# Performance work log

Hardware: AMD Instinct MI355X
Metric: run time of the kernel (lower is better)

## Reference

```python
import jax, jax.numpy as jnp
import numpy as np

B, T, C, H = 32, 512, 8, 256  # batch, seq_len, n_channels, HIDDEN_SIZE
G = 4 * H  # gate dim (i, f, g, o)


def setup_inputs() -> dict:
    key = jax.random.key(0)
    ks = jax.random.split(key, 12)
    k_scale = 1.0 / np.sqrt(H)  # PyTorch LSTM/Linear uniform init bound
    u = lambda k, shape: jax.random.uniform(k, shape, jnp.float32, -k_scale, k_scale)
    return {
        "x": jax.random.normal(ks[0], (B, T, C), jnp.float32),
        # per-channel LSTM layer 1 (input_size=1)
        "Wih1": u(ks[1], (C, G, 1)),
        "Whh1": u(ks[2], (C, G, H)),
        "bih1": u(ks[3], (C, G)),
        "bhh1": u(ks[4], (C, G)),
        # per-channel LSTM layer 2 (input_size=H)
        "Wih2": u(ks[5], (C, G, H)),
        "Whh2": u(ks[6], (C, G, H)),
        "bih2": u(ks[7], (C, G)),
        "bhh2": u(ks[8], (C, G)),
        # per-channel Linear(H, 1)
        "Wlin": u(ks[9], (C, H)),
        "blin": u(ks[10], (C,)),
    }


def _lstm_layer(x_proj, Whh):
    """x_proj: [T, C, B, 4H] precomputed input projection + biases.
    Whh: [C, 4H, H]. Returns hidden states [T, C, B, H]."""
    c_dim, b_dim = x_proj.shape[1], x_proj.shape[2]
    h0 = jnp.zeros((c_dim, b_dim, H), x_proj.dtype)
    c0 = jnp.zeros((c_dim, b_dim, H), x_proj.dtype)

    def step(carry, xp_t):
        h, c = carry
        gates = xp_t + jnp.einsum('cbh,cgh->cbg', h, Whh)
        i, f, g, o = jnp.split(gates, 4, axis=-1)  # PyTorch gate order i,f,g,o
        i = jax.nn.sigmoid(i)
        f = jax.nn.sigmoid(f)
        g = jnp.tanh(g)
        o = jax.nn.sigmoid(o)
        c_new = f * c + i * g
        h_new = o * jnp.tanh(c_new)
        return (h_new, c_new), h_new

    _, hs = jax.lax.scan(step, (h0, c0), x_proj)
    return hs  # [T, C, B, H]


def reference(x, Wih1, Whh1, bih1, bhh1, Wih2, Whh2, bih2, bhh2, Wlin, blin):
    # Dropout layers are identity in eval mode.
    # Layer 1: input_size=1 -> input projection is a per-channel scale of x.
    b1 = (bih1 + bhh1)[None, :, None, :]  # [1, C, 1, 4H]
    xp1 = jnp.einsum('btc,cg->tcbg', x, Wih1[:, :, 0]) + b1  # [T, C, B, 4H]
    h1 = _lstm_layer(xp1, Whh1)  # [T, C, B, H]

    # Layer 2
    b2 = (bih2 + bhh2)[None, :, None, :]
    xp2 = jnp.einsum('tcbh,cgh->tcbg', h1, Wih2) + b2
    h2 = _lstm_layer(xp2, Whh2)  # [T, C, B, H]

    # Per-channel Linear(H, 1), concatenated over channel dim.
    out = jnp.einsum('tcbh,ch->btc', h2, Wlin) + blin[None, None, :]
    return out  # [B, T, C]
```

## Files before the change

kernel.cpp:

```cpp
#include <hip/hip_runtime.h>

#define Bn 32
#define Tn 512
#define Cn 8
#define Hn 256
#define Gn 1024
#define NTHR 256
#define SLC  16
#define NBLK (Cn*2*SLC)
#define K2n  (Hn/2)
#define BUFS 4
#define EXU  (BUFS*Cn*K2n*Bn)
#define GP2  18

typedef __attribute__((ext_vector_type(8))) __bf16 bf16x8;
typedef __attribute__((ext_vector_type(8))) short  short8;
typedef __attribute__((ext_vector_type(4))) float  f32x4;
typedef __attribute__((ext_vector_type(4))) unsigned uintx4;
typedef unsigned long long u64;

__device__ __forceinline__ unsigned bfr(float f) {
    unsigned u = __float_as_uint(f);
    return (u + 0x7fffu + ((u >> 16) & 1u)) >> 16;
}
__device__ __forceinline__ float sigmf(float v)  { return 1.0f / (1.0f + __expf(-v)); }
__device__ __forceinline__ float tanh_f(float v) { return 1.0f - 2.0f / (__expf(2.0f * v) + 1.0f); }

__device__ __forceinline__ f32x4 mf(short8 a, short8 b, f32x4 c) {
    return __builtin_amdgcn_mfma_f32_16x16x32_bf16(
        __builtin_bit_cast(bf16x8, a), __builtin_bit_cast(bf16x8, b), c, 0, 0, 0);
}

__device__ __forceinline__ void splitw(const float* __restrict__ p, short8& hi, short8& lo) {
    short8 h, l;
#pragma unroll
    for (int j = 0; j < 8; ++j) {
        const float v = p[j];
        const unsigned hb = bfr(v);
        h[j] = (short)hb;
        l[j] = (short)bfr(v - __uint_as_float(hb << 16));
    }
    hi = h; lo = l;
}

__device__ __forceinline__ void ast64(u64* p, u64 v) {
    __hip_atomic_store(p, v, __ATOMIC_RELAXED, __HIP_MEMORY_SCOPE_AGENT);
}
__device__ __forceinline__ u64 ald64(const u64* p) {
    return __hip_atomic_load(p, __ATOMIC_RELAXED, __HIP_MEMORY_SCOPE_AGENT);
}

__global__ void __launch_bounds__(NTHR, 1)
lstm_mfma(const float* __restrict__ x,
          const float* __restrict__ Wih1, const float* __restrict__ Whh1,
          const float* __restrict__ bih1, const float* __restrict__ bhh1,
          const float* __restrict__ Wih2, const float* __restrict__ Whh2,
          const float* __restrict__ bih2, const float* __restrict__ bhh2,
          const float* __restrict__ Wlin, const float* __restrict__ blin,
          float* __restrict__ out, void* __restrict__ wsv, int use_part) {
    __shared__ float g1buf[2 * 64 * GP2];
    __shared__ float g2buf[2 * 64 * GP2];

    u64* EX1 = (u64*)wsv;
    u64* EX2 = EX1 + EXU;
    float* part = (float*)(EX2 + EXU);

    const int tid  = threadIdx.x;
    const int wg   = blockIdx.x;
    const int c    = wg & 7;
    const int s    = (wg >> 3) & 15;
    const int bh   = (wg >> 7) & 1;
    const int lane = tid & 63;
    const int wid  = tid >> 6;
    const int kg   = wid & 1;
    const int mh   = wid >> 1;
    const int n    = lane & 15;
    const int quad = lane >> 4;
    const int bn   = bh * 16 + n;

    short8 w1h[2][4], w1l[2][4], w2h[2][4], w2l[2][4], w3h[2][4], w3l[2][4];
#pragma unroll
    for (int mt = 0; mt < 2; ++mt) {
        const int r = mh * 32 + mt * 16 + n;
        const size_t g = (size_t)((r >> 4) * Hn + s * 16 + (r & 15));
        const size_t base = (size_t)c * Gn * Hn + g * Hn + kg * 128 + quad * 8;
#pragma unroll
        for (int kk = 0; kk < 4; ++kk) {
            splitw(Whh1 + base + kk * 32, w1h[mt][kk], w1l[mt][kk]);
            splitw(Wih2 + base + kk * 32, w2h[mt][kk], w2l[mt][kk]);
            splitw(Whh2 + base + kk * 32, w3h[mt][kk], w3l[mt][kk]);
        }
    }

    float wi1_r[2][4], bs1_r[2][4], bs2_r[2][4];
#pragma unroll
    for (int mt = 0; mt < 2; ++mt)
#pragma unroll
        for (int reg = 0; reg < 4; ++reg) {
            const int r = mh * 32 + mt * 16 + quad * 4 + reg;
            const int g = (r >> 4) * Hn + s * 16 + (r & 15);
            wi1_r[mt][reg] = Wih1[c * Gn + g];
            bs1_r[mt][reg] = bih1[c * Gn + g] + bhh1[c * Gn + g];
            bs2_r[mt][reg] = bih2[c * Gn + g] + bhh2[c * Gn + g];
        }

    const int jj = tid & 15;
    const int bb = tid >> 4;
    const int gb = bh * 16 + bb;
    const float wl = Wlin[c * Hn + s * 16 + jj];
    const float bl = blin[c];

    float c1 = 0.0f, c2 = 0.0f;

    for (int t = 0; t <= Tn; ++t) {
        const bool doA = (t < Tn);
        const bool doB = (t >= 1);
        const int wb = t & 3;
        const int rb = (t + 3) & 3;
        const unsigned ctag = (unsigned)(t % 3) + 1u;
        const unsigned ptag = (unsigned)((t + 2) % 3) + 1u;

        const float xv = doA ? x[(bn * Tn + t) * Cn + c] : 0.0f;

        const u64* E1 = EX1 + (size_t)(rb * Cn + c) * K2n * Bn;
        const u64* E2 = EX2 + (size_t)(rb * Cn + c) * K2n * Bn;
        const unsigned em = (ptag & 1u) | ((ptag & 2u) << 15);
        const bool chk1 = (t >= 1);
        const bool chk2 = (t >= 2);
        short8 f2h[4], f2l[4], f1h[4], f1l[4];
        bool got1 = false, got2 = false;
        for (;;) {
            unsigned bad1 = 0, bad2 = 0;
            if (!got2) {
#pragma unroll
                for (int kk = 0; kk < 4; ++kk) {
                    uintx4 a2h, a2l;
#pragma unroll
                    for (int j2 = 0; j2 < 4; ++j2) {
                        const int k2 = kg * 64 + kk * 16 + quad * 4 + j2;
                        const u64 v2 = ald64(E2 + k2 * Bn + bn);
                        a2h[j2] = (unsigned)v2;
                        a2l[j2] = (unsigned)(v2 >> 32);
                        bad2 |= (a2l[j2] ^ em) & 0x00010001u;
                    }
                    f2h[kk] = __builtin_bit_cast(short8, a2h);
                    f2l[kk] = __builtin_bit_cast(short8, a2l);
                }
            }
            if (!got1) {
#pragma unroll
                for (int kk = 0; kk < 4; ++kk) {
                    uintx4 a1h, a1l;
#pragma unroll
                    for (int j2 = 0; j2 < 4; ++j2) {
                        const int k2 = kg * 64 + kk * 16 + quad * 4 + j2;
                        const u64 v1 = ald64(E1 + k2 * Bn + bn);
                        a1h[j2] = (unsigned)v1;
                        a1l[j2] = (unsigned)(v1 >> 32);
                        bad1 |= (a1l[j2] ^ em) & 0x00010001u;
                    }
                    f1h[kk] = __builtin_bit_cast(short8, a1h);
                    f1l[kk] = __builtin_bit_cast(short8, a1l);
                }
            }
            if (!got2) got2 = !chk2 || __all((int)(bad2 == 0));
            if (!got1) got1 = !chk1 || __all((int)(bad1 == 0));
            if (got1 && got2) break;
            __builtin_amdgcn_s_sleep(1);
        }

        f32x4 a1a[2] = {{0,0,0,0},{0,0,0,0}}, a1x[2] = {{0,0,0,0},{0,0,0,0}};
        f32x4 a2a[2] = {{0,0,0,0},{0,0,0,0}}, a2x[2] = {{0,0,0,0},{0,0,0,0}};
#pragma unroll
        for (int kk = 0; kk < 4; ++kk)
#pragma unroll
            for (int mt = 0; mt < 2; ++mt) {
                a2a[mt] = mf(w3h[mt][kk], f2h[kk], a2a[mt]);
                a2x[mt] = mf(w3l[mt][kk], f2h[kk], mf(w3h[mt][kk], f2l[kk], a2x[mt]));
                a1a[mt] = mf(w1h[mt][kk], f1h[kk], a1a[mt]);
                a1x[mt] = mf(w1l[mt][kk], f1h[kk], mf(w1h[mt][kk], f1l[kk], a1x[mt]));
                a2a[mt] = mf(w2h[mt][kk], f1h[kk], a2a[mt]);
                a2x[mt] = mf(w2l[mt][kk], f1h[kk], mf(w2h[mt][kk], f1l[kk], a2x[mt]));
            }

#pragma unroll
        for (int mt = 0; mt < 2; ++mt)
#pragma unroll
            for (int reg = 0; reg < 4; ++reg) {
                const int r = mh * 32 + mt * 16 + quad * 4 + reg;
                const int off = (kg * 64 + r) * GP2 + n;
                float e1 = a1a[mt][reg] + a1x[mt][reg];
                float e2 = a2a[mt][reg] + a2x[mt][reg];
                if (kg == 0) {
                    e1 += xv * wi1_r[mt][reg] + bs1_r[mt][reg];
                    e2 += bs2_r[mt][reg];
                }
                g1buf[off] = e1;
                g2buf[off] = e2;
            }
        __syncthreads();

        const unsigned cm = (ctag & 1u) | ((ctag & 2u) << 15);

        if (doA) {
            const float iv = sigmf (g1buf[jj * GP2 + bb]        + g1buf[(64 + jj) * GP2 + bb]);
            const float fv = sigmf (g1buf[(16 + jj) * GP2 + bb] + g1buf[(80 + jj) * GP2 + bb]);
            const float gv = tanh_f(g1buf[(32 + jj) * GP2 + bb] + g1buf[(96 + jj) * GP2 + bb]);
            const float ov = sigmf (g1buf[(48 + jj) * GP2 + bb] + g1buf[(112 + jj) * GP2 + bb]);
            c1 = fv * c1 + iv * gv;
            const float h1v = ov * tanh_f(c1);
            const unsigned hb = bfr(h1v);
            const unsigned lb = bfr(h1v - __uint_as_float(hb << 16));
            const unsigned packed = (hb << 16) | lb;
            const unsigned nbp = (unsigned)__shfl_xor((int)packed, 1, 64);
            if ((jj & 1) == 0) {
                const unsigned hip = (packed >> 16) | (nbp & 0xffff0000u);
                unsigned lop = (packed & 0xffffu) | (nbp << 16);
                lop = (lop & 0xFFFEFFFEu) | cm;
                const int k2 = s * 8 + (jj >> 1);
                ast64(EX1 + (size_t)(wb * Cn + c) * K2n * Bn + k2 * Bn + gb,
                      (u64)hip | ((u64)lop << 32));
            }
        }
        if (doB) {
            const float iv = sigmf (g2buf[jj * GP2 + bb]        + g2buf[(64 + jj) * GP2 + bb]);
            const float fv = sigmf (g2buf[(16 + jj) * GP2 + bb] + g2buf[(80 + jj) * GP2 + bb]);
            const float gv = tanh_f(g2buf[(32 + jj) * GP2 + bb] + g2buf[(96 + jj) * GP2 + bb]);
            const float ov = sigmf (g2buf[(48 + jj) * GP2 + bb] + g2buf[(112 + jj) * GP2 + bb]);
            c2 = fv * c2 + iv * gv;
            const float h2v = ov * tanh_f(c2);
            if (t < Tn) {
                const unsigned hb = bfr(h2v);
                const unsigned lb = bfr(h2v - __uint_as_float(hb << 16));
                const unsigned packed = (hb << 16) | lb;
                const unsigned nbp = (unsigned)__shfl_xor((int)packed, 1, 64);
                if ((jj & 1) == 0) {
                    const unsigned hip = (packed >> 16) | (nbp & 0xffff0000u);
                    unsigned lop = (packed & 0xffffu) | (nbp << 16);
                    lop = (lop & 0xFFFEFFFEu) | cm;
                    const int k2 = s * 8 + (jj >> 1);
                    ast64(EX2 + (size_t)(wb * Cn + c) * K2n * Bn + k2 * Bn + gb,
                          (u64)hip | ((u64)lop << 32));
                }
            } else {
                (void)__shfl_xor(0, 1, 64);
            }

            float pv = h2v * wl;
            pv += __shfl_xor(pv, 1, 64);
            pv += __shfl_xor(pv, 2, 64);
            pv += __shfl_xor(pv, 4, 64);
            pv += __shfl_xor(pv, 8, 64);
            if (jj == 0) {
                if (use_part) {
                    part[(((t - 1) * Cn + c) * SLC + s) * Bn + gb] = pv;
                } else {
                    atomicAdd(&out[(gb * Tn + (t - 1)) * Cn + c], pv + (s == 0 ? bl : 0.0f));
                }
            }
        }

        __syncthreads();
    }
}

__global__ void reduce_out(const float* __restrict__ part, const float* __restrict__ blin,
                           float* __restrict__ out) {
    const int t = blockIdx.x;
    const int c = threadIdx.x >> 5;
    const int b = threadIdx.x & 31;
    float v = blin[c];
#pragma unroll
    for (int s = 0; s < SLC; ++s) v += part[((t * Cn + c) * SLC + s) * Bn + b];
    out[(b * Tn + t) * Cn + c] = v;
}

extern "C" void kernel_launch(void* const* d_in, const int* in_sizes, int n_in,
                              void* d_out, int out_size, void* d_ws, size_t ws_size,
                              hipStream_t stream) {
    const float* x    = (const float*)d_in[0];
    const float* Wih1 = (const float*)d_in[1];
    const float* Whh1 = (const float*)d_in[2];
    const float* bih1 = (const float*)d_in[3];
    const float* bhh1 = (const float*)d_in[4];
    const float* Wih2 = (const float*)d_in[5];
    const float* Whh2 = (const float*)d_in[6];
    const float* bih2 = (const float*)d_in[7];
    const float* bhh2 = (const float*)d_in[8];
    const float* Wlin = (const float*)d_in[9];
    const float* blin = (const float*)d_in[10];
    float* out = (float*)d_out;

    const size_t h_bytes    = (size_t)2 * EXU * sizeof(u64);
    const size_t part_bytes = (size_t)Tn * Cn * SLC * Bn * sizeof(float);
    const int use_part = (ws_size >= h_bytes + part_bytes) ? 1 : 0;

    hipMemsetAsync(d_ws, 0, h_bytes, stream);
    if (!use_part)
        hipMemsetAsync(d_out, 0, (size_t)out_size * sizeof(float), stream);

    lstm_mfma<<<NBLK, NTHR, 0, stream>>>(
        x, Wih1, Whh1, bih1, bhh1, Wih2, Whh2, bih2, bhh2, Wlin, blin, out, d_ws, use_part);

    if (use_part) {
        const float* part = (const float*)((const char*)d_ws + h_bytes);
        reduce_out<<<Tn, Cn * Bn, 0, stream>>>(part, blin, out);
    }
}
```

Measured before the change: 1.865 ms.

## Decouple layer-2 dependency wait from layer-1 and move Wih2 weights to LDS

Splits the per-step work so layer 1 waits only for h1 exchange, computes and publishes h1 first. Layer 2 then issues its h2 loads, does the Wih2·h1 MFMAs while those loads are in flight, and only afterwards checks h2 readiness before the Whh2 MFMAs. The layer-2 exchange is re-indexed so it publishes one step earlier in the ring, and the Wih2 split weights are moved from registers to shared memory to reduce register pressure. This shortens the critical path across workgroups, at the cost of LDS reads each step and a changed synchronisation structure.

After: 1.960 ms. 5.1% more time.

```diff
diff --git a/kernel.cpp b/kernel.cpp
--- a/kernel.cpp
+++ b/kernel.cpp
@@ -60,6 +60,7 @@
           float* __restrict__ out, void* __restrict__ wsv, int use_part) {
     __shared__ float g1buf[2 * 64 * GP2];
     __shared__ float g2buf[2 * 64 * GP2];
+    __shared__ short8 w2lds[4][2][4][2][64];
 
     u64* EX1 = (u64*)wsv;
     u64* EX2 = EX1 + EXU;
@@ -78,7 +79,7 @@
     const int quad = lane >> 4;
     const int bn   = bh * 16 + n;
 
-    short8 w1h[2][4], w1l[2][4], w2h[2][4], w2l[2][4], w3h[2][4], w3l[2][4];
+    short8 w1h[2][4], w1l[2][4], w3h[2][4], w3l[2][4];
 #pragma unroll
     for (int mt = 0; mt < 2; ++mt) {
         const int r = mh * 32 + mt * 16 + n;
@@ -87,8 +88,11 @@
 #pragma unroll
         for (int kk = 0; kk < 4; ++kk) {
             splitw(Whh1 + base + kk * 32, w1h[mt][kk], w1l[mt][kk]);
-            splitw(Wih2 + base + kk * 32, w2h[mt][kk], w2l[mt][kk]);
             splitw(Whh2 + base + kk * 32, w3h[mt][kk], w3l[mt][kk]);
+            short8 t2h, t2l;
+            splitw(Wih2 + base + kk * 32, t2h, t2l);
+            w2lds[wid][mt][kk][0][lane] = t2h;
+            w2lds[wid][mt][kk][1][lane] = t2l;
         }
     }
 
@@ -110,97 +114,63 @@
     const float wl = Wlin[c * Hn + s * 16 + jj];
     const float bl = blin[c];
 
+    __syncthreads();
+
     float c1 = 0.0f, c2 = 0.0f;
 
     for (int t = 0; t <= Tn; ++t) {
         const bool doA = (t < Tn);
         const bool doB = (t >= 1);
-        const int wb = t & 3;
-        const int rb = (t + 3) & 3;
-        const unsigned ctag = (unsigned)(t % 3) + 1u;
-        const unsigned ptag = (unsigned)((t + 2) % 3) + 1u;
 
         const float xv = doA ? x[(bn * Tn + t) * Cn + c] : 0.0f;
 
-        const u64* E1 = EX1 + (size_t)(rb * Cn + c) * K2n * Bn;
-        const u64* E2 = EX2 + (size_t)(rb * Cn + c) * K2n * Bn;
-        const unsigned em = (ptag & 1u) | ((ptag & 2u) << 15);
-        const bool chk1 = (t >= 1);
-        const bool chk2 = (t >= 2);
-        short8 f2h[4], f2l[4], f1h[4], f1l[4];
-        bool got1 = false, got2 = false;
-        for (;;) {
-            unsigned bad1 = 0, bad2 = 0;
-            if (!got2) {
+        const u64* E1 = EX1 + (size_t)(((t + 3) & 3) * Cn + c) * K2n * Bn;
+        short8 f1h[4], f1l[4];
+        {
+            const unsigned ptag = (unsigned)((t + 2) % 3) + 1u;
+            const unsigned em = (ptag & 1u) | ((ptag & 2u) << 15);
+            const bool chk = (t >= 1);
+            for (;;) {
+                unsigned bad = 0;
 #pragma unroll
                 for (int kk = 0; kk < 4; ++kk) {
-                    uintx4 a2h, a2l;
-#pragma unroll
-                    for (int j2 = 0; j2 < 4; ++j2) {
-                        const int k2 = kg * 64 + kk * 16 + quad * 4 + j2;
-                        const u64 v2 = ald64(E2 + k2 * Bn + bn);
-                        a2h[j2] = (unsigned)v2;
-                        a2l[j2] = (unsigned)(v2 >> 32);
-                        bad2 |= (a2l[j2] ^ em) & 0x00010001u;
-                    }
-                    f2h[kk] = __builtin_bit_cast(short8, a2h);
-                    f2l[kk] = __builtin_bit_cast(short8, a2l);
-                }
-            }
-            if (!got1) {
-#pragma unroll
-                for (int kk = 0; kk < 4; ++kk) {
-                    uintx4 a1h, a1l;
+                    uintx4 ah, al;
 #pragma unroll
                     for (int j2 = 0; j2 < 4; ++j2) {
                         const int k2 = kg * 64 + kk * 16 + quad * 4 + j2;
                         const u64 v1 = ald64(E1 + k2 * Bn + bn);
-                        a1h[j2] = (unsigned)v1;
-                        a1l[j2] = (unsigned)(v1 >> 32);
-                        bad1 |= (a1l[j2] ^ em) & 0x00010001u;
+                        ah[j2] = (unsigned)v1;
+                        al[j2] = (unsigned)(v1 >> 32);
+                        bad |= (al[j2] ^ em) & 0x00010001u;
                     }
-                    f1h[kk] = __builtin_bit_cast(short8, a1h);
-                    f1l[kk] = __builtin_bit_cast(short8, a1l);
-                }
-            }
-            if (!got2) got2 = !chk2 || __all((int)(bad2 == 0));
-            if (!got1) got1 = !chk1 || __all((int)(bad1 == 0));
-            if (got1 && got2) break;
-            __builtin_amdgcn_s_sleep(1);
-        }
-
-        f32x4 a1a[2] = {{0,0,0,0},{0,0,0,0}}, a1x[2] = {{0,0,0,0},{0,0,0,0}};
-        f32x4 a2a[2] = {{0,0,0,0},{0,0,0,0}}, a2x[2] = {{0,0,0,0},{0,0,0,0}};
-#pragma unroll
-        for (int kk = 0; kk < 4; ++kk)
-#pragma unroll
-            for (int mt = 0; mt < 2; ++mt) {
-                a2a[mt] = mf(w3h[mt][kk], f2h[kk], a2a[mt]);
-                a2x[mt] = mf(w3l[mt][kk], f2h[kk], mf(w3h[mt][kk], f2l[kk], a2x[mt]));
-                a1a[mt] = mf(w1h[mt][kk], f1h[kk], a1a[mt]);
-                a1x[mt] = mf(w1l[mt][kk], f1h[kk], mf(w1h[mt][kk], f1l[kk], a1x[mt]));
-                a2a[mt] = mf(w2h[mt][kk], f1h[kk], a2a[mt]);
-                a2x[mt] = mf(w2l[mt][kk], f1h[kk], mf(w2h[mt][kk], f1l[kk], a2x[mt]));
-            }
-
-#pragma unroll
-        for (int mt = 0; mt < 2; ++mt)
-#pragma unroll
-            for (int reg = 0; reg < 4; ++reg) {
-                const int r = mh * 32 + mt * 16 + quad * 4 + reg;
-                const int off = (kg * 64 + r) * GP2 + n;
-                float e1 = a1a[mt][reg] + a1x[mt][reg];
-                float e2 = a2a[mt][reg] + a2x[mt][reg];
-                if (kg == 0) {
-                    e1 += xv * wi1_r[mt][reg] + bs1_r[mt][reg];
-                    e2 += bs2_r[mt][reg];
-                }
-                g1buf[off] = e1;
-                g2buf[off] = e2;
-            }
+                    f1h[kk] = __builtin_bit_cast(short8, ah);
+                    f1l[kk] = __builtin_bit_cast(short8, al);
+                }
+                if (!chk || __all((int)(bad == 0))) break;
+                __builtin_amdgcn_s_sleep(1);
+            }
+        }
+
+        if (doA) {
+            f32x4 a1a[2] = {{0,0,0,0},{0,0,0,0}}, a1x[2] = {{0,0,0,0},{0,0,0,0}};
+#pragma unroll
+            for (int kk = 0; kk < 4; ++kk)
+#pragma unroll
+                for (int mt = 0; mt < 2; ++mt) {
+                    a1a[mt] = mf(w1h[mt][kk], f1h[kk], a1a[mt]);
+                    a1x[mt] = mf(w1l[mt][kk], f1h[kk], mf(w1h[mt][kk], f1l[kk], a1x[mt]));
+                }
+#pragma unroll
+            for (int mt = 0; mt < 2; ++mt)
+#pragma unroll
+                for (int reg = 0; reg < 4; ++reg) {
+                    const int r = mh * 32 + mt * 16 + quad * 4 + reg;
+                    float e1 = a1a[mt][reg] + a1x[mt][reg];
+                    if (kg == 0) e1 += xv * wi1_r[mt][reg] + bs1_r[mt][reg];
+                    g1buf[(kg * 64 + r) * GP2 + n] = e1;
+                }
+        }
         __syncthreads();
-
-        const unsigned cm = (ctag & 1u) | ((ctag & 2u) << 15);
 
         if (doA) {
             const float iv = sigmf (g1buf[jj * GP2 + bb]        + g1buf[(64 + jj) * GP2 + bb]);
@@ -213,15 +183,94 @@
             const unsigned lb = bfr(h1v - __uint_as_float(hb << 16));
             const unsigned packed = (hb << 16) | lb;
             const unsigned nbp = (unsigned)__shfl_xor((int)packed, 1, 64);
+            const unsigned ctag = (unsigned)(t % 3) + 1u;
+            const unsigned cm = (ctag & 1u) | ((ctag & 2u) << 15);
             if ((jj & 1) == 0) {
                 const unsigned hip = (packed >> 16) | (nbp & 0xffff0000u);
                 unsigned lop = (packed & 0xffffu) | (nbp << 16);
                 lop = (lop & 0xFFFEFFFEu) | cm;
                 const int k2 = s * 8 + (jj >> 1);
-                ast64(EX1 + (size_t)(wb * Cn + c) * K2n * Bn + k2 * Bn + gb,
+                ast64(EX1 + (size_t)((t & 3) * Cn + c) * K2n * Bn + k2 * Bn + gb,
                       (u64)hip | ((u64)lop << 32));
             }
         }
+
+        const u64* E2 = EX2 + (size_t)(((t + 2) & 3) * Cn + c) * K2n * Bn;
+        u64 r2[4][4];
+        if (doB) {
+#pragma unroll
+            for (int kk = 0; kk < 4; ++kk)
+#pragma unroll
+                for (int j2 = 0; j2 < 4; ++j2) {
+                    const int k2 = kg * 64 + kk * 16 + quad * 4 + j2;
+                    r2[kk][j2] = ald64(E2 + k2 * Bn + bn);
+                }
+        }
+
+        f32x4 a2a[2] = {{0,0,0,0},{0,0,0,0}}, a2x[2] = {{0,0,0,0},{0,0,0,0}};
+        if (doB) {
+#pragma unroll
+            for (int kk = 0; kk < 4; ++kk)
+#pragma unroll
+                for (int mt = 0; mt < 2; ++mt) {
+                    const short8 wh = w2lds[wid][mt][kk][0][lane];
+                    const short8 wlo = w2lds[wid][mt][kk][1][lane];
+                    a2a[mt] = mf(wh, f1h[kk], a2a[mt]);
+                    a2x[mt] = mf(wlo, f1h[kk], mf(wh, f1l[kk], a2x[mt]));
+                }
+        }
+
+        short8 f2h[4], f2l[4];
+        if (doB) {
+            const unsigned ptag = (unsigned)((t + 1) % 3) + 1u;
+            const unsigned em = (ptag & 1u) | ((ptag & 2u) << 15);
+            const bool chk = (t >= 2);
+            for (;;) {
+                unsigned bad = 0;
+#pragma unroll
+                for (int kk = 0; kk < 4; ++kk) {
+                    uintx4 ah, al;
+#pragma unroll
+                    for (int j2 = 0; j2 < 4; ++j2) {
+                        ah[j2] = (unsigned)r2[kk][j2];
+                        al[j2] = (unsigned)(r2[kk][j2] >> 32);
+                        bad |= (al[j2] ^ em) & 0x00010001u;
+                    }
+                    f2h[kk] = __builtin_bit_cast(short8, ah);
+                    f2l[kk] = __builtin_bit_cast(short8, al);
+                }
+                if (!chk || __all((int)(bad == 0))) break;
+                __builtin_amdgcn_s_sleep(1);
+#pragma unroll
+                for (int kk = 0; kk < 4; ++kk)
+#pragma unroll
+                    for (int j2 = 0; j2 < 4; ++j2) {
+                        const int k2 = kg * 64 + kk * 16 + quad * 4 + j2;
+                        r2[kk][j2] = ald64(E2 + k2 * Bn + bn);
+                    }
+            }
+        }
+
+        if (doB) {
+#pragma unroll
+            for (int kk = 0; kk < 4; ++kk)
+#pragma unroll
+                for (int mt = 0; mt < 2; ++mt) {
+                    a2a[mt] = mf(w3h[mt][kk], f2h[kk], a2a[mt]);
+                    a2x[mt] = mf(w3l[mt][kk], f2h[kk], mf(w3h[mt][kk], f2l[kk], a2x[mt]));
+                }
+#pragma unroll
+            for (int mt = 0; mt < 2; ++mt)
+#pragma unroll
+                for (int reg = 0; reg < 4; ++reg) {
+                    const int r = mh * 32 + mt * 16 + quad * 4 + reg;
+                    float e2 = a2a[mt][reg] + a2x[mt][reg];
+                    if (kg == 0) e2 += bs2_r[mt][reg];
+                    g2buf[(kg * 64 + r) * GP2 + n] = e2;
+                }
+        }
+        __syncthreads();
+
         if (doB) {
             const float iv = sigmf (g2buf[jj * GP2 + bb]        + g2buf[(64 + jj) * GP2 + bb]);
             const float fv = sigmf (g2buf[(16 + jj) * GP2 + bb] + g2buf[(80 + jj) * GP2 + bb]);
@@ -229,21 +278,19 @@
             const float ov = sigmf (g2buf[(48 + jj) * GP2 + bb] + g2buf[(112 + jj) * GP2 + bb]);
             c2 = fv * c2 + iv * gv;
             const float h2v = ov * tanh_f(c2);
-            if (t < Tn) {
-                const unsigned hb = bfr(h2v);
-                const unsigned lb = bfr(h2v - __uint_as_float(hb << 16));
-                const unsigned packed = (hb << 16) | lb;
-                const unsigned nbp = (unsigned)__shfl_xor((int)packed, 1, 64);
-                if ((jj & 1) == 0) {
-                    const unsigned hip = (packed >> 16) | (nbp & 0xffff0000u);
-                    unsigned lop = (packed & 0xffffu) | (nbp << 16);
-                    lop = (lop & 0xFFFEFFFEu) | cm;
-                    const int k2 = s * 8 + (jj >> 1);
-                    ast64(EX2 + (size_t)(wb * Cn + c) * K2n * Bn + k2 * Bn + gb,
-                          (u64)hip | ((u64)lop << 32));
-                }
-            } else {
-                (void)__shfl_xor(0, 1, 64);
+            const unsigned hb = bfr(h2v);
+            const unsigned lb = bfr(h2v - __uint_as_float(hb << 16));
+            const unsigned packed = (hb << 16) | lb;
+            const unsigned nbp = (unsigned)__shfl_xor((int)packed, 1, 64);
+            const unsigned ctag = (unsigned)((t + 2) % 3) + 1u;
+            const unsigned cm = (ctag & 1u) | ((ctag & 2u) << 15);
+            if (t < Tn && (jj & 1) == 0) {
+                const unsigned hip = (packed >> 16) | (nbp & 0xffff0000u);
+                unsigned lop = (packed & 0xffffu) | (nbp << 16);
+                lop = (lop & 0xFFFEFFFEu) | cm;
+                const int k2 = s * 8 + (jj >> 1);
+                ast64(EX2 + (size_t)(((t + 3) & 3) * Cn + c) * K2n * Bn + k2 * Bn + gb,
+                      (u64)hip | ((u64)lop << 32));
             }
 
             float pv = h2v * wl;
@@ -259,8 +306,6 @@
                 }
             }
         }
-
-        __syncthreads();
     }
 }
 
```
